# Kernel tuning notes

Measured on AMD Instinct MI355X. Metric: run time of the kernel, lower is better.

Reference implementation:

```python
import jax, jax.numpy as jnp
import numpy as np

B, S, IN, H, OUT = 32, 512, 1024, 1024, 1024


def setup_inputs() -> dict:
    key = jax.random.key(0)
    ks = jax.random.split(key, 12)
    sc = 0.02
    d = {
        "x": jax.random.normal(ks[0], (B, S, IN), dtype=jnp.float32),
        # torch nn.Linear weights are (out_features, in_features); in_features = IN + H
        "Wf": jax.random.normal(ks[1], (H, IN + H), dtype=jnp.float32) * sc,
        "bf": jax.random.normal(ks[2], (H,), dtype=jnp.float32) * sc,
        "Wi": jax.random.normal(ks[3], (H, IN + H), dtype=jnp.float32) * sc,
        "bi": jax.random.normal(ks[4], (H,), dtype=jnp.float32) * sc,
        "Wc": jax.random.normal(ks[5], (H, IN + H), dtype=jnp.float32) * sc,
        "bc": jax.random.normal(ks[6], (H,), dtype=jnp.float32) * sc,
        "Wo": jax.random.normal(ks[7], (H, IN + H), dtype=jnp.float32) * sc,
        "bo": jax.random.normal(ks[8], (H,), dtype=jnp.float32) * sc,
        "Wfc": jax.random.normal(ks[9], (OUT, H), dtype=jnp.float32) * sc,
        "bfc": jax.random.normal(ks[10], (OUT,), dtype=jnp.float32) * sc,
    }
    return d


def reference(x, Wf, bf, Wi, bi, Wc, bc, Wo, bo, Wfc, bfc):
    batch, seq_len, _ = x.shape
    hidden = Wf.shape[0]
    h0 = jnp.zeros((batch, hidden), dtype=x.dtype)
    c0 = jnp.zeros((batch, hidden), dtype=x.dtype)

    def step(carry, x_t):
        h, c = carry
        # NOTE: original concatenates (h_t, x_t) in this order
        z = jnp.concatenate([h, x_t], axis=1)  # [B, H+IN]
        f = jax.nn.sigmoid(z @ Wf.T + bf)
        i = jax.nn.sigmoid(z @ Wi.T + bi)
        c_hat = jnp.tanh(z @ Wc.T + bc)
        c_new = i * c_hat + f * c
        o = jax.nn.sigmoid(z @ Wo.T + bo)
        h_new = o * jnp.tanh(c_new)
        return (h_new, c_new), h_new

    xs = jnp.swapaxes(x, 0, 1)  # [S, B, IN]
    _, hs = jax.lax.scan(step, (h0, c0), xs)  # hs: [S, B, H]
    outputs = jnp.swapaxes(hs, 0, 1)  # [B, S, H]
    out = outputs @ Wfc.T + bfc  # [B, S, OUT]
    return out
```

## Files before the change

### kernel.cpp

```cpp
#include <hip/hip_runtime.h>
#include <hip/hip_bf16.h>

#define BATCH 32
#define SEQ   512
#define IND   1024
#define HD    1024
#define ZD    2048
#define NG    4096
#define WG_ELEMS (1024 * 2048)
#define PBLK 128

typedef short  shortx8 __attribute__((ext_vector_type(8)));
typedef float  floatx4 __attribute__((ext_vector_type(4)));

#define MFMA16(a, b, c) __builtin_amdgcn_mfma_f32_16x16x32_bf16((a), (b), (c), 0, 0, 0)

__device__ __forceinline__ float sigmoidf_(float x) {
    return 1.0f / (1.0f + __expf(-x));
}
__device__ __forceinline__ float tanhf_(float x) {
    return 1.0f - 2.0f / (__expf(2.0f * x) + 1.0f);
}

__device__ __forceinline__ short bf16s(float x) {
    __hip_bfloat16 h = __float2bfloat16(x);
    return *reinterpret_cast<short*>(&h);
}

__device__ __forceinline__ float bf2f(unsigned short u) {
    unsigned v = ((unsigned)u) << 16;
    float f;
    __builtin_memcpy(&f, &v, 4);
    return f;
}

__device__ __forceinline__ shortx8 cvt8(const float* __restrict__ p) {
    float4 v0 = *(const float4*)p;
    float4 v1 = *(const float4*)(p + 4);
    shortx8 r;
    r[0] = bf16s(v0.x); r[1] = bf16s(v0.y); r[2] = bf16s(v0.z); r[3] = bf16s(v0.w);
    r[4] = bf16s(v1.x); r[5] = bf16s(v1.y); r[6] = bf16s(v1.z); r[7] = bf16s(v1.w);
    return r;
}

__global__ __launch_bounds__(256) void cvt_f32_bf16(
    const float* __restrict__ src, __hip_bfloat16* __restrict__ dst, int n)
{
    int i = (blockIdx.x * 256 + threadIdx.x) * 4;
    if (i < n) {
        float4 v = *(const float4*)(src + i);
        dst[i + 0] = __float2bfloat16(v.x);
        dst[i + 1] = __float2bfloat16(v.y);
        dst[i + 2] = __float2bfloat16(v.z);
        dst[i + 3] = __float2bfloat16(v.w);
    }
}

__global__ __launch_bounds__(256) void gemm_gx(
    const float* __restrict__ x,
    const __hip_bfloat16* __restrict__ Wb,
    const float* __restrict__ bf_, const float* __restrict__ bi_,
    const float* __restrict__ bc_, const float* __restrict__ bo_,
    __hip_bfloat16* __restrict__ Gx, const int t0)
{
    const int wave = (blockIdx.x << 2) + (threadIdx.x >> 6);
    const int mt = wave >> 6;
    const int nt = wave & 63;
    const int lane = threadIdx.x & 63;
    const int quad = lane >> 4;
    const int l16  = lane & 15;
    const int m0 = mt << 6;
    const int n0 = nt << 6;
    const int g  = n0 >> 10;
    const __hip_bfloat16* Wg = Wb + (size_t)g * WG_ELEMS;
    const float* bg = (g == 0) ? bf_ : (g == 1) ? bi_ : (g == 2) ? bc_ : bo_;
    const int j0 = n0 & 1023;

    floatx4 acc[4][4];
#pragma unroll
    for (int i = 0; i < 4; i++)
#pragma unroll
        for (int j = 0; j < 4; j++) acc[i][j] = (floatx4)(0.0f);

    const float* arow[4];
    const __hip_bfloat16* brow[4];
#pragma unroll
    for (int i = 0; i < 4; i++) {
        const int r = m0 + i * 16 + l16;
        const int t = t0 + (r >> 5);
        const int b = r & 31;
        arow[i] = x + ((size_t)b * SEQ + t) * IND + quad * 8;
    }
#pragma unroll
    for (int j = 0; j < 4; j++)
        brow[j] = Wg + (size_t)(j0 + j * 16 + l16) * ZD + HD + quad * 8;

    for (int k0 = 0; k0 < IND; k0 += 32) {
        shortx8 a[4], b[4];
#pragma unroll
        for (int i = 0; i < 4; i++) a[i] = cvt8(arow[i] + k0);
#pragma unroll
        for (int j = 0; j < 4; j++) b[j] = *(const shortx8*)(brow[j] + k0);
#pragma unroll
        for (int i = 0; i < 4; i++)
#pragma unroll
            for (int j = 0; j < 4; j++)
                acc[i][j] = MFMA16(a[i], b[j], acc[i][j]);
    }

#pragma unroll
    for (int j = 0; j < 4; j++) {
        const int n  = n0 + j * 16 + l16;
        const int jj = j0 + j * 16 + l16;
        const float bias = bg[jj];
#pragma unroll
        for (int i = 0; i < 4; i++) {
#pragma unroll
            for (int r = 0; r < 4; r++) {
                const int row = m0 + i * 16 + quad * 4 + r;
                Gx[(size_t)row * NG + n] = __float2bfloat16(acc[i][j][r] + bias);
            }
        }
    }
}

__global__ __launch_bounds__(256) void lstm_step(
    const __hip_bfloat16* __restrict__ gx,
    const int t,
    const __hip_bfloat16* __restrict__ Wb,
    const __hip_bfloat16* __restrict__ hzero,
    float* __restrict__ c,
    __hip_bfloat16* __restrict__ hs)
{
    const int jt = (blockIdx.x << 2) + (threadIdx.x >> 6);
    const int lane = threadIdx.x & 63;
    const int quad = lane >> 4;
    const int l16  = lane & 15;
    const int j0   = jt << 4;

    const __hip_bfloat16* hb;
    size_t rstride;
    if (t == 0) { hb = hzero; rstride = HD; }
    else        { hb = hs + (size_t)(t - 1) * HD; rstride = (size_t)SEQ * HD; }

    const __hip_bfloat16* wrow[4];
#pragma unroll
    for (int g = 0; g < 4; g++)
        wrow[g] = Wb + (size_t)g * WG_ELEMS + (size_t)(j0 + l16) * ZD + quad * 8;

    const __hip_bfloat16* hrow0 = hb + (size_t)l16 * rstride + quad * 8;
    const __hip_bfloat16* hrow1 = hb + (size_t)(16 + l16) * rstride + quad * 8;

    floatx4 acc[4][2];
#pragma unroll
    for (int g = 0; g < 4; g++) { acc[g][0] = (floatx4)(0.0f); acc[g][1] = (floatx4)(0.0f); }

    for (int k0 = 0; k0 < HD; k0 += 32) {
        shortx8 a0 = *(const shortx8*)(hrow0 + k0);
        shortx8 a1 = *(const shortx8*)(hrow1 + k0);
#pragma unroll
        for (int g = 0; g < 4; g++) {
            shortx8 bfrag = *(const shortx8*)(wrow[g] + k0);
            acc[g][0] = MFMA16(a0, bfrag, acc[g][0]);
            acc[g][1] = MFMA16(a1, bfrag, acc[g][1]);
        }
    }

    const int j = j0 + l16;
#pragma unroll
    for (int i = 0; i < 2; i++) {
#pragma unroll
        for (int r = 0; r < 4; r++) {
            const int bb = i * 16 + quad * 4 + r;
            const size_t gbase = (size_t)bb * NG + j;
            const float fp = acc[0][i][r] + __bfloat162float(gx[gbase + 0 * HD]);
            const float ip = acc[1][i][r] + __bfloat162float(gx[gbase + 1 * HD]);
            const float cp = acc[2][i][r] + __bfloat162float(gx[gbase + 2 * HD]);
            const float op = acc[3][i][r] + __bfloat162float(gx[gbase + 3 * HD]);
            const float fg = sigmoidf_(fp);
            const float ig = sigmoidf_(ip);
            const float cg = tanhf_(cp);
            const float og = sigmoidf_(op);
            const size_t ci = (size_t)bb * HD + j;
            const float cnew = ig * cg + fg * c[ci];
            const float hnew = og * tanhf_(cnew);
            c[ci] = cnew;
            hs[((size_t)bb * SEQ + t) * HD + j] = __float2bfloat16(hnew);
        }
    }
}

__global__ __launch_bounds__(256, 1) void lstm_persist(
    const __hip_bfloat16* __restrict__ Wb,
    const float* __restrict__ x,
    __hip_bfloat16* __restrict__ Gx,
    const float* __restrict__ bf_, const float* __restrict__ bi_,
    const float* __restrict__ bc_, const float* __restrict__ bo_,
    const __hip_bfloat16* __restrict__ Wfcb,
    const float* __restrict__ bfc,
    float* __restrict__ out,
    const int T,
    const __hip_bfloat16* __restrict__ hzero,
    float* __restrict__ c_ws,
    __hip_bfloat16* __restrict__ hs,
    unsigned* __restrict__ bar)
{
    __shared__ float accf[2 * 1168];

    const int tid  = threadIdx.x;
    const int blk  = blockIdx.x;
    const int wv   = tid >> 6;
    const int lane = tid & 63;
    const int quad = lane >> 4;
    const int l16  = lane & 15;
    unsigned* gcnt = bar + 2048;

    if (blk >= PBLK) {
        const int pb_ = blk - PBLK;
        const int pw = pb_ * 4 + wv;
        {
            const int nt = pw & 63;
            const int n0 = nt << 6;
            const int g  = n0 >> 10;
            const __hip_bfloat16* Wg = Wb + (size_t)g * WG_ELEMS;
            const float* bg = (g == 0) ? bf_ : (g == 1) ? bi_ : (g == 2) ? bc_ : bo_;
            const int j0 = n0 & 1023;

            const __hip_bfloat16* brow[4];
#pragma unroll
            for (int j = 0; j < 4; j++)
                brow[j] = Wg + (size_t)(j0 + j * 16 + l16) * ZD + HD + quad * 8;

            float bias[4];
#pragma unroll
            for (int j = 0; j < 4; j++) bias[j] = bg[j0 + j * 16 + l16];

            for (int it = 0; it < 32; it++) {
                const int mt = (pw >> 6) + 8 * it;
                const int m0 = mt << 6;

                floatx4 acc[4][4];
#pragma unroll
                for (int i = 0; i < 4; i++)
#pragma unroll
                    for (int j = 0; j < 4; j++) acc[i][j] = (floatx4)(0.0f);

                const float* arow[4];
#pragma unroll
                for (int i = 0; i < 4; i++) {
                    const int r = m0 + i * 16 + l16;
                    const int t = r >> 5;
                    const int b = r & 31;
                    arow[i] = x + ((size_t)b * SEQ + t) * IND + quad * 8;
                }

                for (int k0 = 0; k0 < IND; k0 += 32) {
                    shortx8 a[4], b[4];
#pragma unroll
                    for (int i = 0; i < 4; i++) a[i] = cvt8(arow[i] + k0);
#pragma unroll
                    for (int j = 0; j < 4; j++) b[j] = *(const shortx8*)(brow[j] + k0);
#pragma unroll
                    for (int i = 0; i < 4; i++)
#pragma unroll
                        for (int j = 0; j < 4; j++)
                            acc[i][j] = MFMA16(a[i], b[j], acc[i][j]);
                }

#pragma unroll
                for (int j = 0; j < 4; j++) {
                    const int n = n0 + j * 16 + l16;
#pragma unroll
                    for (int i = 0; i < 4; i++) {
#pragma unroll
                        for (int r = 0; r < 4; r++) {
                            const int row = m0 + i * 16 + quad * 4 + r;
                            const float v = acc[i][j][r] + bias[j];
                            const unsigned my = (unsigned)(unsigned short)bf16s(v);
                            const unsigned nb = (unsigned)__shfl_xor((int)my, 1);
                            if ((l16 & 1) == 0) {
                                unsigned* dst = (unsigned*)(Gx + (size_t)row * NG + n);
                                __hip_atomic_store(dst, my | (nb << 16),
                                                   __ATOMIC_RELAXED,
                                                   __HIP_MEMORY_SCOPE_AGENT);
                            }
                        }
                    }
                }
                asm volatile("s_waitcnt vmcnt(0)" ::: "memory");
                if (lane == 0)
                    __hip_atomic_fetch_add(gcnt + mt * 16, 1u,
                                           __ATOMIC_RELAXED, __HIP_MEMORY_SCOPE_AGENT);
            }
        }

        {
            const int fb  = (pb_ & 7) * 4 + wv;
            const int fnt = pb_ >> 3;
            const int n0  = fnt << 6;

            const __hip_bfloat16* brow[4];
#pragma unroll
            for (int j = 0; j < 4; j++)
                brow[j] = Wfcb + (size_t)(n0 + j * 16 + l16) * HD + quad * 8;
            float biasf[4];
#pragma unroll
            for (int j = 0; j < 4; j++) biasf[j] = bfc[n0 + j * 16 + l16];

            for (int tc = 0; tc < 8; tc++) {
                const unsigned need = (unsigned)((tc + 1) * 64);
                {
                    unsigned* p0 = bar + lane * 16;
                    unsigned* p1 = bar + (64 + lane) * 16;
                    bool d0 = false, d1 = false;
                    while (true) {
                        if (!d0) d0 = (__hip_atomic_load(p0, __ATOMIC_RELAXED,
                                           __HIP_MEMORY_SCOPE_AGENT) >= need);
                        if (!d1) d1 = (__hip_atomic_load(p1, __ATOMIC_RELAXED,
                                           __HIP_MEMORY_SCOPE_AGENT) >= need);
                        if (__all(d0 && d1)) break;
                        __builtin_amdgcn_s_sleep(8);
                    }
                    asm volatile("" ::: "memory");
                    __builtin_amdgcn_sched_barrier(0);
                }

                const int m0 = fb * SEQ + tc * 64;

                floatx4 acc[4][4];
#pragma unroll
                for (int i = 0; i < 4; i++)
#pragma unroll
                    for (int j = 0; j < 4; j++) acc[i][j] = (floatx4)(0.0f);

                const __hip_bfloat16* arow[4];
#pragma unroll
                for (int i = 0; i < 4; i++)
                    arow[i] = hs + (size_t)(m0 + i * 16 + l16) * HD + quad * 8;

                for (int k0 = 0; k0 < HD; k0 += 32) {
                    shortx8 a[4], b[4];
#pragma unroll
                    for (int i = 0; i < 4; i++) a[i] = *(const shortx8*)(arow[i] + k0);
#pragma unroll
                    for (int j = 0; j < 4; j++) b[j] = *(const shortx8*)(brow[j] + k0);
#pragma unroll
                    for (int i = 0; i < 4; i++)
#pragma unroll
                        for (int j = 0; j < 4; j++)
                            acc[i][j] = MFMA16(a[i], b[j], acc[i][j]);
                }

#pragma unroll
                for (int j = 0; j < 4; j++) {
                    const int n = n0 + j * 16 + l16;
#pragma unroll
                    for (int i = 0; i < 4; i++) {
#pragma unroll
                        for (int r = 0; r < 4; r++) {
                            const int row = m0 + i * 16 + quad * 4 + r;
                            out[(size_t)row * 1024 + n] = acc[i][j][r] + biasf[j];
                        }
                    }
                }
            }
        }
        return;
    }

    const int wm = wv & 1;
    const int wk = wv >> 1;

    shortx8 Bfrag[2][16];
#pragma unroll
    for (int ct = 0; ct < 2; ct++) {
        const int lc = ct * 16 + l16;
        const int jj = lc >> 2, g = lc & 3;
        const __hip_bfloat16* wr =
            Wb + (size_t)g * WG_ELEMS + (size_t)(blk * 8 + jj) * ZD + wk * 512 + quad * 8;
#pragma unroll
        for (int ks = 0; ks < 16; ks++)
            Bfrag[ct][ks] = *(const shortx8*)(wr + ks * 32);
    }

    const int pjj = tid & 7;
    const int pb  = tid >> 3;
    const int pj  = blk * 8 + pjj;
    float creg = c_ws[blk * 256 + tid];

    while (__hip_atomic_load(gcnt, __ATOMIC_RELAXED,
                             __HIP_MEMORY_SCOPE_AGENT) < 64)
        __builtin_amdgcn_s_sleep(1);
    asm volatile("" ::: "memory");
    __builtin_amdgcn_sched_barrier(0);

    unsigned short gxr0, gxr1, gxr2, gxr3;
    {
        const __hip_bfloat16* gx = Gx + (size_t)pb * NG + pj;
        gxr0 = *(const unsigned short*)(gx + 0 * HD);
        gxr1 = *(const unsigned short*)(gx + 1 * HD);
        gxr2 = *(const unsigned short*)(gx + 2 * HD);
        gxr3 = *(const unsigned short*)(gx + 3 * HD);
    }
    int mt_ok = 0;

    for (int tt = 0; tt < T; tt++) {
        const int t = tt;
        const __hip_bfloat16* hb;
        size_t rstride;
        if (t == 0) { hb = hzero; rstride = HD; }
        else        { hb = hs + (size_t)(t - 1) * HD; rstride = (size_t)SEQ * HD; }

        unsigned short ngxr0 = 0, ngxr1 = 0, ngxr2 = 0, ngxr3 = 0;
        if (tt + 1 < T) {
            const int mtn = (tt + 1) >> 1;
            if (mtn > mt_ok) {
                while (__hip_atomic_load(gcnt + mtn * 16, __ATOMIC_RELAXED,
                                         __HIP_MEMORY_SCOPE_AGENT) < 64)
                    __builtin_amdgcn_s_sleep(1);
                mt_ok = mtn;
                asm volatile("" ::: "memory");
                __builtin_amdgcn_sched_barrier(0);
            }
            const __hip_bfloat16* gx1 = Gx + ((size_t)(tt + 1) * BATCH + pb) * NG + pj;
            ngxr0 = *(const unsigned short*)(gx1 + 0 * HD);
            ngxr1 = *(const unsigned short*)(gx1 + 1 * HD);
            ngxr2 = *(const unsigned short*)(gx1 + 2 * HD);
            ngxr3 = *(const unsigned short*)(gx1 + 3 * HD);
        }

        const __hip_bfloat16* arow =
            hb + (size_t)(wm * 16 + l16) * rstride + wk * 512 + quad * 8;
        floatx4 acc0 = (floatx4)(0.0f), acc1 = (floatx4)(0.0f);
#pragma unroll
        for (int ks = 0; ks < 16; ks++) {
            shortx8 av = *(const shortx8*)(arow + ks * 32);
            acc0 = MFMA16(av, Bfrag[0][ks], acc0);
            acc1 = MFMA16(av, Bfrag[1][ks], acc1);
        }

        {
            const int b0 = wm * 16 + quad * 4;
            *(floatx4*)(accf + wk * 1168 + (l16)      * 36 + b0) = acc0;
            *(floatx4*)(accf + wk * 1168 + (16 + l16) * 36 + b0) = acc1;
        }
        __syncthreads();

        {
            const int i0 = (pjj * 4 + 0) * 36 + pb;
            const int i1 = (pjj * 4 + 1) * 36 + pb;
            const int i2 = (pjj * 4 + 2) * 36 + pb;
            const int i3 = (pjj * 4 + 3) * 36 + pb;
            const float fp = accf[i0] + accf[1168 + i0] + bf2f(gxr0);
            const float ip = accf[i1] + accf[1168 + i1] + bf2f(gxr1);
            const float cp = accf[i2] + accf[1168 + i2] + bf2f(gxr2);
            const float op = accf[i3] + accf[1168 + i3] + bf2f(gxr3);
            const float fg = sigmoidf_(fp);
            const float ig = sigmoidf_(ip);
            const float cg = tanhf_(cp);
            const float og = sigmoidf_(op);
            creg = ig * cg + fg * creg;
            const float hnew = og * tanhf_(creg);

            const unsigned my = (unsigned)(unsigned short)bf16s(hnew);
            const unsigned nb = (unsigned)__shfl_xor((int)my, 1);
            if ((tid & 1) == 0) {
                unsigned* dst = (unsigned*)(hs + ((size_t)pb * SEQ + t) * HD + pj);
                const unsigned packed = my | (nb << 16);
                __hip_atomic_store(dst, packed, __ATOMIC_RELAXED,
                                   __HIP_MEMORY_SCOPE_AGENT);
            }
        }

        __syncthreads();
        if (wv == 0 && lane == 0) {
            __hip_atomic_store(bar + blk * 16, (unsigned)(tt + 1),
                               __ATOMIC_RELAXED, __HIP_MEMORY_SCOPE_AGENT);
        }
        if (tt < T - 1) {
            const unsigned epoch = (unsigned)(tt + 1);
            if (wv == 0) {
                unsigned* p0 = bar + lane * 16;
                unsigned* p1 = bar + (64 + lane) * 16;
                bool d0 = false, d1 = false;
                while (true) {
                    if (!d0) d0 = (__hip_atomic_load(p0, __ATOMIC_RELAXED,
                                       __HIP_MEMORY_SCOPE_AGENT) >= epoch);
                    if (!d1) d1 = (__hip_atomic_load(p1, __ATOMIC_RELAXED,
                                       __HIP_MEMORY_SCOPE_AGENT) >= epoch);
                    if (__all(d0 && d1)) break;
                    __builtin_amdgcn_s_sleep(1);
                }
                asm volatile("" ::: "memory");
                __builtin_amdgcn_sched_barrier(0);
            }
            __syncthreads();
        }

        gxr0 = ngxr0; gxr1 = ngxr1; gxr2 = ngxr2; gxr3 = ngxr3;
    }

    c_ws[blk * 256 + tid] = creg;
}

__global__ __launch_bounds__(256) void gemm_fc(
    const __hip_bfloat16* __restrict__ hs,
    const __hip_bfloat16* __restrict__ Wfcb,
    const float* __restrict__ bfc,
    float* __restrict__ out)
{
    const int wave = (blockIdx.x << 2) + (threadIdx.x >> 6);
    const int mt = wave >> 4;
    const int nt = wave & 15;
    const int lane = threadIdx.x & 63;
    const int quad = lane >> 4;
    const int l16  = lane & 15;
    const int m0 = mt << 6;
    const int n0 = nt << 6;

    floatx4 acc[4][4];
#pragma unroll
    for (int i = 0; i < 4; i++)
#pragma unroll
        for (int j = 0; j < 4; j++) acc[i][j] = (floatx4)(0.0f);

    const __hip_bfloat16* arow[4];
    const __hip_bfloat16* brow[4];
#pragma unroll
    for (int i = 0; i < 4; i++)
        arow[i] = hs + (size_t)(m0 + i * 16 + l16) * HD + quad * 8;
#pragma unroll
    for (int j = 0; j < 4; j++)
        brow[j] = Wfcb + (size_t)(n0 + j * 16 + l16) * HD + quad * 8;

    for (int k0 = 0; k0 < HD; k0 += 32) {
        shortx8 a[4], b[4];
#pragma unroll
        for (int i = 0; i < 4; i++) a[i] = *(const shortx8*)(arow[i] + k0);
#pragma unroll
        for (int j = 0; j < 4; j++) b[j] = *(const shortx8*)(brow[j] + k0);
#pragma unroll
        for (int i = 0; i < 4; i++)
#pragma unroll
            for (int j = 0; j < 4; j++)
                acc[i][j] = MFMA16(a[i], b[j], acc[i][j]);
    }

#pragma unroll
    for (int j = 0; j < 4; j++) {
        const int n = n0 + j * 16 + l16;
        const float bias = bfc[n];
#pragma unroll
        for (int i = 0; i < 4; i++) {
#pragma unroll
            for (int r = 0; r < 4; r++) {
                const int row = m0 + i * 16 + quad * 4 + r;
                out[(size_t)row * 1024 + n] = acc[i][j][r] + bias;
            }
        }
    }
}

extern "C" void kernel_launch(void* const* d_in, const int* in_sizes, int n_in,
                              void* d_out, int out_size, void* d_ws, size_t ws_size,
                              hipStream_t stream) {
    const float* x   = (const float*)d_in[0];
    const float* Wf  = (const float*)d_in[1];
    const float* bf_ = (const float*)d_in[2];
    const float* Wi  = (const float*)d_in[3];
    const float* bi_ = (const float*)d_in[4];
    const float* Wc  = (const float*)d_in[5];
    const float* bc_ = (const float*)d_in[6];
    const float* Wo  = (const float*)d_in[7];
    const float* bo_ = (const float*)d_in[8];
    const float* Wfc = (const float*)d_in[9];
    const float* bfc = (const float*)d_in[10];
    float* out = (float*)d_out;

    char* ws = (char*)d_ws;
    const size_t WB_OFF  = 0;
    const size_t WFC_OFF = (size_t)4 * WG_ELEMS * 2;
    const size_t HS_OFF  = WFC_OFF + (size_t)HD * HD * 2;
    const size_t ST_OFF  = HS_OFF + (size_t)BATCH * SEQ * HD * 2;
    const size_t HZ_BYTES  = (size_t)BATCH * HD * 2;
    const size_t C_BYTES   = (size_t)PBLK * 256 * 4;
    const size_t BAR_BYTES = 128 * 64 + 256 * 64;
    const size_t ST_BYTES  = HZ_BYTES + C_BYTES + BAR_BYTES;
    const size_t GX_OFF  = ST_OFF + ST_BYTES;

    __hip_bfloat16* Wb    = (__hip_bfloat16*)(ws + WB_OFF);
    __hip_bfloat16* Wfcb  = (__hip_bfloat16*)(ws + WFC_OFF);
    __hip_bfloat16* hs    = (__hip_bfloat16*)(ws + HS_OFF);
    __hip_bfloat16* hzero = (__hip_bfloat16*)(ws + ST_OFF);
    float*          cbuf  = (float*)(ws + ST_OFF + HZ_BYTES);
    unsigned*       bar   = (unsigned*)(ws + ST_OFF + HZ_BYTES + C_BYTES);
    __hip_bfloat16* Gx    = (__hip_bfloat16*)(ws + GX_OFF);

    const size_t GX_FULL = (size_t)SEQ * BATCH * NG * 2;
    const int persist = (GX_OFF + GX_FULL <= ws_size);
    int T_CHUNK = 1;
    if (!persist) {
        const size_t GX_STEP = (size_t)BATCH * NG * 2;
        const int fopts[3] = {8, 2, 1};
        for (int i = 0; i < 3; i++) {
            if (GX_OFF + (size_t)fopts[i] * GX_STEP <= ws_size) {
                T_CHUNK = fopts[i]; break;
            }
        }
    }

    cvt_f32_bf16<<<2048, 256, 0, stream>>>(Wf, Wb + 0 * (size_t)WG_ELEMS, WG_ELEMS);
    cvt_f32_bf16<<<2048, 256, 0, stream>>>(Wi, Wb + 1 * (size_t)WG_ELEMS, WG_ELEMS);
    cvt_f32_bf16<<<2048, 256, 0, stream>>>(Wc, Wb + 2 * (size_t)WG_ELEMS, WG_ELEMS);
    cvt_f32_bf16<<<2048, 256, 0, stream>>>(Wo, Wb + 3 * (size_t)WG_ELEMS, WG_ELEMS);
    cvt_f32_bf16<<<1024, 256, 0, stream>>>(Wfc, Wfcb, HD * HD);

    hipMemsetAsync(ws + ST_OFF, 0, ST_BYTES, stream);

    if (persist) {
        lstm_persist<<<2 * PBLK, 256, 0, stream>>>(
            Wb, x, Gx, bf_, bi_, bc_, bo_, Wfcb, bfc, out,
            SEQ, hzero, cbuf, hs, bar);
    } else {
        for (int t0 = 0; t0 < SEQ; t0 += T_CHUNK) {
            gemm_gx<<<T_CHUNK * 8, 256, 0, stream>>>(
                x, Wb, bf_, bi_, bc_, bo_, Gx, t0);
            for (int t = t0; t < t0 + T_CHUNK; t++) {
                const __hip_bfloat16* gx_t = Gx + (size_t)(t - t0) * BATCH * NG;
                lstm_step<<<16, 256, 0, stream>>>(gx_t, t, Wb, hzero, cbuf, hs);
            }
        }
        gemm_fc<<<1024, 256, 0, stream>>>(hs, Wfcb, bfc, out);
    }
}
```

Baseline: 2.754 ms.

## Replace global all-block barrier with per-dependency flag waits, pad flags, fuse weight casts

The recurrent step loop no longer has every block wait for all 128 blocks' step flags after each step. Each wave now waits only on the single producer flag for the k-slice of h it reads (mywatch), so the global barrier becomes point-to-point dependencies. Flag counters are padded to a 68-word stride to cut false sharing and channel hotspots, and the FC and initial waits now spin in one wave and then use __syncthreads. The five weight-conversion launches are merged into one kernel to remove launch overhead. The changes add correctness risk around the relaxed-ordering visibility of h, relying on the existing store/flag protocol.

```diff
diff --git a/kernel.cpp b/kernel.cpp
--- a/kernel.cpp
+++ b/kernel.cpp
@@ -9,6 +9,7 @@
 #define NG    4096
 #define WG_ELEMS (1024 * 2048)
 #define PBLK 128
+#define FSTR 68
 
 typedef short  shortx8 __attribute__((ext_vector_type(8)));
 typedef float  floatx4 __attribute__((ext_vector_type(4)));
@@ -43,17 +44,29 @@
     return r;
 }
 
-__global__ __launch_bounds__(256) void cvt_f32_bf16(
-    const float* __restrict__ src, __hip_bfloat16* __restrict__ dst, int n)
+__global__ __launch_bounds__(256) void cvt_weights(
+    const float* __restrict__ Wf, const float* __restrict__ Wi,
+    const float* __restrict__ Wc, const float* __restrict__ Wo,
+    const float* __restrict__ Wfc,
+    __hip_bfloat16* __restrict__ Wb, __hip_bfloat16* __restrict__ Wfcb)
 {
-    int i = (blockIdx.x * 256 + threadIdx.x) * 4;
-    if (i < n) {
-        float4 v = *(const float4*)(src + i);
-        dst[i + 0] = __float2bfloat16(v.x);
-        dst[i + 1] = __float2bfloat16(v.y);
-        dst[i + 2] = __float2bfloat16(v.z);
-        dst[i + 3] = __float2bfloat16(v.w);
-    }
+    int b = blockIdx.x;
+    const float* src;
+    __hip_bfloat16* dst;
+    if (b < 8192) {
+        const int g = b >> 11;
+        src = (g == 0) ? Wf : (g == 1) ? Wi : (g == 2) ? Wc : Wo;
+        dst = Wb + (size_t)g * WG_ELEMS;
+        b &= 2047;
+    } else {
+        src = Wfc; dst = Wfcb; b -= 8192;
+    }
+    const int i = (b * 256 + threadIdx.x) * 4;
+    float4 v = *(const float4*)(src + i);
+    dst[i + 0] = __float2bfloat16(v.x);
+    dst[i + 1] = __float2bfloat16(v.y);
+    dst[i + 2] = __float2bfloat16(v.z);
+    dst[i + 3] = __float2bfloat16(v.w);
 }
 
 __global__ __launch_bounds__(256) void gemm_gx(
@@ -213,7 +226,7 @@
     const int lane = tid & 63;
     const int quad = lane >> 4;
     const int l16  = lane & 15;
-    unsigned* gcnt = bar + 2048;
+    unsigned* gcnt = bar + 128 * FSTR;
 
     if (blk >= PBLK) {
         const int pb_ = blk - PBLK;
@@ -289,7 +302,7 @@
                 }
                 asm volatile("s_waitcnt vmcnt(0)" ::: "memory");
                 if (lane == 0)
-                    __hip_atomic_fetch_add(gcnt + mt * 16, 1u,
+                    __hip_atomic_fetch_add(gcnt + (size_t)mt * FSTR, 1u,
                                            __ATOMIC_RELAXED, __HIP_MEMORY_SCOPE_AGENT);
             }
         }
@@ -309,9 +322,9 @@
 
             for (int tc = 0; tc < 8; tc++) {
                 const unsigned need = (unsigned)((tc + 1) * 64);
-                {
-                    unsigned* p0 = bar + lane * 16;
-                    unsigned* p1 = bar + (64 + lane) * 16;
+                if (wv == 0) {
+                    unsigned* p0 = bar + (size_t)lane * FSTR;
+                    unsigned* p1 = bar + (size_t)(64 + lane) * FSTR;
                     bool d0 = false, d1 = false;
                     while (true) {
                         if (!d0) d0 = (__hip_atomic_load(p0, __ATOMIC_RELAXED,
@@ -324,6 +337,7 @@
                     asm volatile("" ::: "memory");
                     __builtin_amdgcn_sched_barrier(0);
                 }
+                __syncthreads();
 
                 const int m0 = fb * SEQ + tc * 64;
 
@@ -388,11 +402,14 @@
     const int pj  = blk * 8 + pjj;
     float creg = c_ws[blk * 256 + tid];
 
-    while (__hip_atomic_load(gcnt, __ATOMIC_RELAXED,
-                             __HIP_MEMORY_SCOPE_AGENT) < 64)
-        __builtin_amdgcn_s_sleep(1);
-    asm volatile("" ::: "memory");
-    __builtin_amdgcn_sched_barrier(0);
+    if (wv == 0) {
+        while (__hip_atomic_load(gcnt, __ATOMIC_RELAXED,
+                                 __HIP_MEMORY_SCOPE_AGENT) < 64)
+            __builtin_amdgcn_s_sleep(1);
+        asm volatile("" ::: "memory");
+        __builtin_amdgcn_sched_barrier(0);
+    }
+    __syncthreads();
 
     unsigned short gxr0, gxr1, gxr2, gxr3;
     {
@@ -404,6 +421,8 @@
     }
     int mt_ok = 0;
 
+    unsigned* mywatch = bar + (size_t)(wk * 64 + lane) * FSTR;
+
     for (int tt = 0; tt < T; tt++) {
         const int t = tt;
         const __hip_bfloat16* hb;
@@ -415,7 +434,7 @@
         if (tt + 1 < T) {
             const int mtn = (tt + 1) >> 1;
             if (mtn > mt_ok) {
-                while (__hip_atomic_load(gcnt + mtn * 16, __ATOMIC_RELAXED,
+                while (__hip_atomic_load(gcnt + (size_t)mtn * FSTR, __ATOMIC_RELAXED,
                                          __HIP_MEMORY_SCOPE_AGENT) < 64)
                     __builtin_amdgcn_s_sleep(1);
                 mt_ok = mtn;
@@ -427,6 +446,14 @@
             ngxr1 = *(const unsigned short*)(gx1 + 1 * HD);
             ngxr2 = *(const unsigned short*)(gx1 + 2 * HD);
             ngxr3 = *(const unsigned short*)(gx1 + 3 * HD);
+        }
+
+        if (tt > 0) {
+            while (__hip_atomic_load(mywatch, __ATOMIC_RELAXED,
+                                     __HIP_MEMORY_SCOPE_AGENT) < (unsigned)tt)
+                __builtin_amdgcn_s_sleep(1);
+            asm volatile("" ::: "memory");
+            __builtin_amdgcn_sched_barrier(0);
         }
 
         const __hip_bfloat16* arow =
@@ -474,27 +501,8 @@
 
         __syncthreads();
         if (wv == 0 && lane == 0) {
-            __hip_atomic_store(bar + blk * 16, (unsigned)(tt + 1),
+            __hip_atomic_store(bar + (size_t)blk * FSTR, (unsigned)(tt + 1),
                                __ATOMIC_RELAXED, __HIP_MEMORY_SCOPE_AGENT);
-        }
-        if (tt < T - 1) {
-            const unsigned epoch = (unsigned)(tt + 1);
-            if (wv == 0) {
-                unsigned* p0 = bar + lane * 16;
-                unsigned* p1 = bar + (64 + lane) * 16;
-                bool d0 = false, d1 = false;
-                while (true) {
-                    if (!d0) d0 = (__hip_atomic_load(p0, __ATOMIC_RELAXED,
-                                       __HIP_MEMORY_SCOPE_AGENT) >= epoch);
-                    if (!d1) d1 = (__hip_atomic_load(p1, __ATOMIC_RELAXED,
-                                       __HIP_MEMORY_SCOPE_AGENT) >= epoch);
-                    if (__all(d0 && d1)) break;
-                    __builtin_amdgcn_s_sleep(1);
-                }
-                asm volatile("" ::: "memory");
-                __builtin_amdgcn_sched_barrier(0);
-            }
-            __syncthreads();
         }
 
         gxr0 = ngxr0; gxr1 = ngxr1; gxr2 = ngxr2; gxr3 = ngxr3;
@@ -584,7 +592,7 @@
     const size_t ST_OFF  = HS_OFF + (size_t)BATCH * SEQ * HD * 2;
     const size_t HZ_BYTES  = (size_t)BATCH * HD * 2;
     const size_t C_BYTES   = (size_t)PBLK * 256 * 4;
-    const size_t BAR_BYTES = 128 * 64 + 256 * 64;
+    const size_t BAR_BYTES = (size_t)(128 + 256) * FSTR * 4;
     const size_t ST_BYTES  = HZ_BYTES + C_BYTES + BAR_BYTES;
     const size_t GX_OFF  = ST_OFF + ST_BYTES;
 
@@ -609,11 +617,7 @@
         }
     }
 
-    cvt_f32_bf16<<<2048, 256, 0, stream>>>(Wf, Wb + 0 * (size_t)WG_ELEMS, WG_ELEMS);
-    cvt_f32_bf16<<<2048, 256, 0, stream>>>(Wi, Wb + 1 * (size_t)WG_ELEMS, WG_ELEMS);
-    cvt_f32_bf16<<<2048, 256, 0, stream>>>(Wc, Wb + 2 * (size_t)WG_ELEMS, WG_ELEMS);
-    cvt_f32_bf16<<<2048, 256, 0, stream>>>(Wo, Wb + 3 * (size_t)WG_ELEMS, WG_ELEMS);
-    cvt_f32_bf16<<<1024, 256, 0, stream>>>(Wfc, Wfcb, HD * HD);
+    cvt_weights<<<9216, 256, 0, stream>>>(Wf, Wi, Wc, Wo, Wfc, Wb, Wfcb);
 
     hipMemsetAsync(ws + ST_OFF, 0, ST_BYTES, stream);
 
```

New measurement: 2.389 ms (median of 2 runs). 13.2% less time.
